# Kernel tuning notes

Measured on AMD Instinct MI355X. Metric: run time of the kernel, lower is better.

## Reference

```python
import jax, jax.numpy as jnp
import numpy as np

B = 8
S_MAX = 1024
H = 12
HD = 64
D = H * HD
DFF = 4 * D
NEG = -1.0e9  # matches Triton kernel's -1000000000.0 mask value


def _layernorm(x, g, b, eps=1e-6):
    mu = jnp.mean(x, axis=-1, keepdims=True)
    var = jnp.mean((x - mu) ** 2, axis=-1, keepdims=True)
    return (x - mu) * jax.lax.rsqrt(var + eps) * g + b


def setup_inputs() -> dict:
    key = jax.random.key(0)
    ks = jax.random.split(key, 12)
    lengths = np.array([1024, 896, 768, 640, 896, 1024, 512, 384], dtype=np.int32)
    assert lengths.max() <= S_MAX and len(lengths) == B
    total = int(lengths.sum())  # 6144
    cu = jnp.asarray(np.concatenate([[0], np.cumsum(lengths)]), dtype=jnp.int32)
    s = 0.02
    return {
        "x": jax.random.normal(ks[0], (total, D), jnp.float32),
        "cu_seqlens": cu,
        "g1": jnp.ones((D,), jnp.float32),
        "beta1": jnp.zeros((D,), jnp.float32),
        "Wqkv": jax.random.normal(ks[1], (D, 3 * D), jnp.float32) * s,
        "bqkv": jnp.zeros((3 * D,), jnp.float32),
        "Wo": jax.random.normal(ks[2], (D, D), jnp.float32) * s,
        "bo": jnp.zeros((D,), jnp.float32),
        "g2": jnp.ones((D,), jnp.float32),
        "beta2": jnp.zeros((D,), jnp.float32),
        "W1": jax.random.normal(ks[3], (D, DFF), jnp.float32) * s,
        "b_fc1": jnp.zeros((DFF,), jnp.float32),
        "W2": jax.random.normal(ks[4], (DFF, D), jnp.float32) * s,
        "b_fc2": jnp.zeros((D,), jnp.float32),
    }


def _ragged_attention(q, k, v, cu_seqlens):
    # q,k,v: [Total, H, HD] packed ragged sequences; cu_seqlens: [B+1] int32
    total = q.shape[0]
    lens = cu_seqlens[1:] - cu_seqlens[:-1]                      # [B]
    s = jnp.arange(S_MAX)
    pad_idx = cu_seqlens[:-1, None] + jnp.minimum(s[None, :], lens[:, None] - 1)  # [B,S]
    valid = s[None, :] < lens[:, None]                           # [B,S]
    qp = q[pad_idx]                                              # [B,S,H,HD]
    kp = k[pad_idx]
    vp = v[pad_idx]
    scale = 1.0 / jnp.sqrt(jnp.float32(HD))
    scores = jnp.einsum("bqhd,bkhd->bhqk", qp, kp) * scale      # [B,H,S,S]
    scores = jnp.where(valid[:, None, None, :], scores, NEG)     # mask invalid keys
    p = jax.nn.softmax(scores, axis=-1)
    op = jnp.einsum("bhqk,bkhd->bqhd", p, vp)                   # [B,S,H,HD]
    # repack to [Total, H, HD]
    tok = jnp.arange(total)
    seg = jnp.searchsorted(cu_seqlens, tok, side="right") - 1    # sequence id per token
    pos = tok - cu_seqlens[seg]
    return op[seg, pos]


def _forward(x, cu_seqlens, g1, beta1, Wqkv, bqkv, Wo, bo, g2, beta2, W1, b_fc1, W2, b_fc2):
    total = x.shape[0]
    qkv = (_layernorm(x, g1, beta1) @ Wqkv + bqkv).reshape(total, 3, H, HD)
    q, k, v = qkv[:, 0], qkv[:, 1], qkv[:, 2]
    attn = _ragged_attention(q, k, v, cu_seqlens).reshape(total, D)
    x = x + (attn @ Wo + bo)                                     # proj_drop/ls1/drop_path identity (eval)
    h = _layernorm(x, g2, beta2)
    m = jax.nn.gelu(h @ W1 + b_fc1, approximate=False)
    return x + (m @ W2 + b_fc2)


def reference(x, cu_seqlens, g1, beta1, Wqkv, bqkv, Wo, bo, g2, beta2, W1, b_fc1, W2, b_fc2):
    return _forward(x, cu_seqlens, g1, beta1, Wqkv, bqkv, Wo, bo, g2, beta2, W1, b_fc1, W2, b_fc2)
```

## Files before the change

kernel.cpp:

```cpp
#include <hip/hip_runtime.h>
#include <hip/hip_bf16.h>
#include <stdint.h>
#include <string.h>

#define D_MODEL 768
#define H_HEADS 12
#define HD_ 64
#define N_QKV 2304

typedef __bf16 bf16x8 __attribute__((ext_vector_type(8)));
typedef float f32x4 __attribute__((ext_vector_type(4)));
typedef __attribute__((address_space(3))) char lds_char;

__device__ __forceinline__ unsigned short f2bfbits(float f) {
  union { float f; unsigned u; } x; x.f = f;
  unsigned r = x.u + 0x7fffu + ((x.u >> 16) & 1u);
  return (unsigned short)(r >> 16);
}

__device__ __forceinline__ unsigned pk2(float a, float b) {
  union { float f; unsigned u; } x, y; x.f = a; y.f = b;
  return ((x.u + 0x8000u) >> 16) | ((y.u + 0x8000u) & 0xffff0000u);
}

__device__ __forceinline__ void gload_lds16(const void* g, void* l) {
  __builtin_amdgcn_global_load_lds(
      (const __attribute__((address_space(1))) unsigned int*)g,
      (__attribute__((address_space(3))) unsigned int*)l, 16, 0, 0);
}

#define DSR(dst, ptr, IMM) \
  asm volatile("ds_read_b128 %0, %1 offset:%2" : "=v"(dst) : "v"(ptr), "n"(IMM))

#define FENCE_() __builtin_amdgcn_sched_barrier(0)
__device__ __forceinline__ void store_sync() {
  FENCE_();
  asm volatile("s_waitcnt lgkmcnt(0)");
  FENCE_();
  __builtin_amdgcn_s_barrier();
  FENCE_();
}

__global__ void transpose_w(const float* __restrict__ in, unsigned short* __restrict__ out,
                            int R, int C) {
  __shared__ float tile[32][33];
  int c0 = blockIdx.x * 32, r0 = blockIdx.y * 32;
  int tx = threadIdx.x, ty = threadIdx.y;
#pragma unroll
  for (int i = 0; i < 32; i += 8)
    tile[ty + i][tx] = in[(size_t)(r0 + ty + i) * C + c0 + tx];
  __syncthreads();
#pragma unroll
  for (int i = 0; i < 32; i += 8)
    out[(size_t)(c0 + ty + i) * R + r0 + tx] = f2bfbits(tile[tx][ty + i]);
}

__global__ void transpose_v(const unsigned short* __restrict__ qkv,
                            unsigned short* __restrict__ vT, int M) {
  __shared__ unsigned short tile[32][33];
  int t0 = blockIdx.x * 32, c0 = blockIdx.y * 32;
  int tx = threadIdx.x, ty = threadIdx.y;
#pragma unroll
  for (int i = 0; i < 32; i += 8)
    tile[ty + i][tx] = qkv[(size_t)(t0 + ty + i) * N_QKV + 1536 + c0 + tx];
  __syncthreads();
  int t = t0 + tx;
  int c = t & 63;
  int kp = ((c >> 5) << 5) | (((c >> 2) & 3) << 3) | (((c >> 4) & 1) << 2) | (c & 3);
  size_t col = (size_t)(t & ~63) + kp;
#pragma unroll
  for (int i = 0; i < 32; i += 8)
    vT[(size_t)(c0 + ty + i) * M + col] = tile[tx][ty + i];
}

__global__ void ln_bf16(const float* __restrict__ x, const float* __restrict__ g,
                        const float* __restrict__ be, unsigned short* __restrict__ out) {
  int row = blockIdx.x;
  const float* xr = x + (size_t)row * D_MODEL;
  int t = threadIdx.x;
  float v0 = xr[t], v1 = xr[t + 256], v2 = xr[t + 512];
  float s = v0 + v1 + v2;
  float s2 = v0 * v0 + v1 * v1 + v2 * v2;
#pragma unroll
  for (int off = 32; off > 0; off >>= 1) {
    s += __shfl_down(s, off, 64);
    s2 += __shfl_down(s2, off, 64);
  }
  __shared__ float red[8];
  int w = t >> 6, lane = t & 63;
  if (lane == 0) { red[w] = s; red[w + 4] = s2; }
  __syncthreads();
  if (t == 0) {
    float a = red[0] + red[1] + red[2] + red[3];
    float b = red[4] + red[5] + red[6] + red[7];
    red[0] = a * (1.0f / 768.0f);
    red[4] = b * (1.0f / 768.0f);
  }
  __syncthreads();
  float mu = red[0];
  float var = red[4] - mu * mu;
  float rs = rsqrtf(var + 1e-6f);
  unsigned short* orow = out + (size_t)row * D_MODEL;
  orow[t]       = f2bfbits((v0 - mu) * rs * g[t]       + be[t]);
  orow[t + 256] = f2bfbits((v1 - mu) * rs * g[t + 256] + be[t + 256]);
  orow[t + 512] = f2bfbits((v2 - mu) * rs * g[t + 512] + be[t + 512]);
}

template <int EPI>
__global__ void __launch_bounds__(256, 3)
gemm_rs(const unsigned short* __restrict__ A,
        const unsigned short* __restrict__ Bt,
        const float* __restrict__ bias,
        const float* __restrict__ res,
        void* __restrict__ outv,
        int M, int N, int K) {
  __shared__ unsigned short lA[2][128 * 32];
  __shared__ unsigned short lB[2][128 * 32];
  int tid = threadIdx.x;
  int w = tid >> 6, lane = tid & 63;
  int id = blockIdx.x;
  int nn = N >> 7, bandM = (M >> 7) >> 3;
  int xcd = id & 7, s = id >> 3;
  int mt = xcd * bandM + s / nn;
  int nt = s - (s / nn) * nn;
  int m0 = mt * 128, n0 = nt * 128;
  int wm = (w >> 1) * 64, wn = (w & 1) * 64;
  f32x4 acc[4][4];
#pragma unroll
  for (int i = 0; i < 4; i++)
#pragma unroll
    for (int j = 0; j < 4; j++) acc[i][j] = (f32x4){0.f, 0.f, 0.f, 0.f};

  int fm = lane & 15, fg = lane >> 4;

  int r0s = w * 16 + (lane >> 2);
  int sc0 = (lane & 3) ^ ((r0s >> 1) & 3);
  const unsigned short* gAs = A + (size_t)(m0 + r0s) * K + sc0 * 8;
  const unsigned short* gBs = Bt + (size_t)(n0 + r0s) * K + sc0 * 8;
  char* lA0 = (char*)&lA[0][0];
  char* lB0 = (char*)&lB[0][0];
  int wo = w * 1024;
  int nk = K >> 5;

  auto stage = [&](int kt, int buf) {
    int kk = kt < nk ? kt : nk - 1;
    int off = kk * 32;
    gload_lds16(gAs + off,                  lA0 + buf * 8192 + wo);
    gload_lds16(gAs + off + (size_t)64 * K, lA0 + buf * 8192 + 4096 + wo);
    gload_lds16(gBs + off,                  lB0 + buf * 8192 + wo);
    gload_lds16(gBs + off + (size_t)64 * K, lB0 + buf * 8192 + 4096 + wo);
  };

  const unsigned aoff0 = (unsigned)((wm + fm) * 64 + ((((wm + fm) >> 1) & 3) ^ fg) * 16);
  const unsigned boff0 = (unsigned)((wn + fm) * 64 + ((((wn + fm) >> 1) & 3) ^ fg) * 16);

  stage(0, 0);
  stage(1, 1);

  for (int k = 0; k < nk; ++k) {
    int cur = k & 1;
    asm volatile("s_waitcnt vmcnt(4)");
    FENCE_();
    __builtin_amdgcn_s_barrier();
    FENCE_();
    bf16x8 af[4], bfr[4];
    const lds_char* pa = (const lds_char*)(lA0 + cur * 8192 + aoff0);
    const lds_char* pb = (const lds_char*)(lB0 + cur * 8192 + boff0);
    DSR(af[0], pa, 0); DSR(af[1], pa, 1024); DSR(af[2], pa, 2048); DSR(af[3], pa, 3072);
    DSR(bfr[0], pb, 0); DSR(bfr[1], pb, 1024); DSR(bfr[2], pb, 2048); DSR(bfr[3], pb, 3072);
    asm volatile("s_waitcnt lgkmcnt(0)");
    FENCE_();
    __builtin_amdgcn_s_barrier();
    FENCE_();
    stage(k + 2, cur);
    FENCE_();
#pragma unroll
    for (int i = 0; i < 4; ++i)
#pragma unroll
      for (int j = 0; j < 4; ++j)
        acc[i][j] = __builtin_amdgcn_mfma_f32_16x16x32_bf16(af[i], bfr[j], acc[i][j], 0, 0, 0);
  }
  asm volatile("s_waitcnt vmcnt(0)");
  FENCE_();

  int er = (lane >> 4) * 4, ec = lane & 15;
#pragma unroll
  for (int i = 0; i < 4; i++) {
#pragma unroll
    for (int j = 0; j < 4; j++) {
      int n = n0 + wn + j * 16 + ec;
      float bv = bias[n];
#pragma unroll
      for (int r = 0; r < 4; r++) {
        int m = m0 + wm + i * 16 + er + r;
        float v = acc[i][j][r] + bv;
        if (EPI == 1) {
          v += res[(size_t)m * N + n];
          ((float*)outv)[(size_t)m * N + n] = v;
        } else {
          if (EPI == 2) v = 0.5f * v * (1.0f + erff(v * 0.70710678118f));
          ((unsigned short*)outv)[(size_t)m * N + n] = f2bfbits(v);
        }
      }
    }
  }
}

template <int EPI>
__global__ void __launch_bounds__(256, 4)
gemm_n64(const unsigned short* __restrict__ A,
         const unsigned short* __restrict__ Bt,
         const float* __restrict__ bias,
         const float* __restrict__ res,
         void* __restrict__ outv,
         int M, int N, int K) {
  __shared__ unsigned short lA[2][128 * 32];
  __shared__ unsigned short lB[2][64 * 32];
  int tid = threadIdx.x;
  int w = tid >> 6, lane = tid & 63;
  int id = blockIdx.x;
  int nn = N >> 6, bandM = (M >> 7) >> 3;
  int xcd = id & 7, s = id >> 3;
  int mt = xcd * bandM + s / nn;
  int nt = s - (s / nn) * nn;
  int m0 = mt * 128, n0 = nt * 64;
  int wm = w * 32;
  f32x4 acc[2][4];
#pragma unroll
  for (int i = 0; i < 2; i++)
#pragma unroll
    for (int j = 0; j < 4; j++) acc[i][j] = (f32x4){0.f, 0.f, 0.f, 0.f};

  int fm = lane & 15, fg = lane >> 4;

  int r0s = w * 16 + (lane >> 2);
  int sc0 = (lane & 3) ^ ((r0s >> 1) & 3);
  const unsigned short* gAs = A + (size_t)(m0 + r0s) * K + sc0 * 8;
  const unsigned short* gBs = Bt + (size_t)(n0 + r0s) * K + sc0 * 8;
  char* lA0 = (char*)&lA[0][0];
  char* lB0 = (char*)&lB[0][0];
  int wo = w * 1024;
  int nk = K >> 5;

  auto stage = [&](int kt, int buf) {
    int kk = kt < nk ? kt : nk - 1;
    int off = kk * 32;
    gload_lds16(gAs + off,                  lA0 + buf * 8192 + wo);
    gload_lds16(gAs + off + (size_t)64 * K, lA0 + buf * 8192 + 4096 + wo);
    gload_lds16(gBs + off,                  lB0 + buf * 4096 + wo);
  };

  const unsigned aoff0 = (unsigned)((wm + fm) * 64 + ((((wm + fm) >> 1) & 3) ^ fg) * 16);
  const unsigned boff0 = (unsigned)(fm * 64 + (((fm >> 1) & 3) ^ fg) * 16);

  stage(0, 0);
  stage(1, 1);

  for (int k = 0; k < nk; ++k) {
    int cur = k & 1;
    asm volatile("s_waitcnt vmcnt(3)");
    FENCE_();
    __builtin_amdgcn_s_barrier();
    FENCE_();
    bf16x8 af[2], bfr[4];
    const lds_char* pa = (const lds_char*)(lA0 + cur * 8192 + aoff0);
    const lds_char* pb = (const lds_char*)(lB0 + cur * 4096 + boff0);
    DSR(af[0], pa, 0); DSR(af[1], pa, 1024);
    DSR(bfr[0], pb, 0); DSR(bfr[1], pb, 1024); DSR(bfr[2], pb, 2048); DSR(bfr[3], pb, 3072);
    asm volatile("s_waitcnt lgkmcnt(0)");
    FENCE_();
    __builtin_amdgcn_s_barrier();
    FENCE_();
    stage(k + 2, cur);
    FENCE_();
#pragma unroll
    for (int i = 0; i < 2; ++i)
#pragma unroll
      for (int j = 0; j < 4; ++j)
        acc[i][j] = __builtin_amdgcn_mfma_f32_16x16x32_bf16(af[i], bfr[j], acc[i][j], 0, 0, 0);
  }
  asm volatile("s_waitcnt vmcnt(0)");
  FENCE_();

  int er = (lane >> 4) * 4, ec = lane & 15;
#pragma unroll
  for (int i = 0; i < 2; i++) {
#pragma unroll
    for (int j = 0; j < 4; j++) {
      int n = n0 + j * 16 + ec;
      float bv = bias[n];
#pragma unroll
      for (int r = 0; r < 4; r++) {
        int m = m0 + wm + i * 16 + er + r;
        float v = acc[i][j][r] + bv;
        if (EPI == 1) {
          v += res[(size_t)m * N + n];
          ((float*)outv)[(size_t)m * N + n] = v;
        } else {
          if (EPI == 2) v = 0.5f * v * (1.0f + erff(v * 0.70710678118f));
          ((unsigned short*)outv)[(size_t)m * N + n] = f2bfbits(v);
        }
      }
    }
  }
}

__global__ void attn_flash4(const unsigned short* __restrict__ qkv,
                            const unsigned short* __restrict__ vT,
                            const int* __restrict__ cu,
                            unsigned short* __restrict__ out, int M) {
  int id = blockIdx.x;
  int qc = id / 96;
  int bh = id - qc * 96;
  int b = bh / 12, h = bh - b * 12;
  int tok0 = cu[b];
  int len = cu[b + 1] - tok0;
  if (qc * 128 >= len) return;

  __shared__ unsigned short lK[2][64 * 64];
  __shared__ unsigned short lVT[2][64 * 64];

  int tid = threadIdx.x, w = tid >> 6, lane = tid & 63;
  int fm = lane & 15, fg = lane >> 4;
  int xm = fm & 7;
  int qbase = qc * 128 + w * 32;

  bf16x8 qf[2][2];
#pragma unroll
  for (int qs = 0; qs < 2; qs++)
#pragma unroll
    for (int kh = 0; kh < 2; kh++)
      qf[qs][kh] = *(const bf16x8*)(qkv + (size_t)(tok0 + qbase + qs * 16 + fm) * N_QKV +
                                    h * 64 + kh * 32 + fg * 8);

  f32x4 Oacc[2][4];
#pragma unroll
  for (int qs = 0; qs < 2; qs++)
#pragma unroll
    for (int dt = 0; dt < 4; dt++) Oacc[qs][dt] = (f32x4){0.f, 0.f, 0.f, 0.f};
  float lrow[2] = {0.f, 0.f};
  const float C2 = 0.18033688011112042f;

  int sr = tid >> 3, sp = tid & 7, sl = sp ^ (sr & 7);
  const unsigned short* kg0 = qkv + D_MODEL + h * 64 + sl * 8;
  const unsigned short* vg0 = vT + (size_t)(h * 64 + sr) * M + tok0 + sl * 8;

  uint4 rk0, rk1, rv0, rv1;
  auto gload = [&](int kt) {
    rk0 = *(const uint4*)(kg0 + (size_t)(tok0 + kt + sr) * N_QKV);
    rk1 = *(const uint4*)(kg0 + (size_t)(tok0 + kt + sr + 32) * N_QKV);
    rv0 = *(const uint4*)(vg0 + kt);
    rv1 = *(const uint4*)(vg0 + (size_t)32 * M + kt);
  };

  int nkt = len >> 6;
  gload(0);
  for (int kt = 0; kt < nkt; kt++) {
    int cur = kt & 1;
    *(uint4*)((char*)&lK[cur][0] + tid * 16) = rk0;
    *(uint4*)((char*)&lK[cur][0] + tid * 16 + 4096) = rk1;
    *(uint4*)((char*)&lVT[cur][0] + tid * 16) = rv0;
    *(uint4*)((char*)&lVT[cur][0] + tid * 16 + 4096) = rv1;
    if (kt + 1 < nkt) gload((kt + 1) * 64);
    store_sync();

    f32x4 s[2][4];
#pragma unroll
    for (int qs = 0; qs < 2; qs++)
#pragma unroll
      for (int t = 0; t < 4; t++) s[qs][t] = (f32x4){0.f, 0.f, 0.f, 0.f};
#pragma unroll
    for (int t = 0; t < 4; t++) {
      bf16x8 kf0 = *(const bf16x8*)&lK[cur][(t * 16 + fm) * 64 + ((fg ^ xm) * 8)];
      bf16x8 kf1 = *(const bf16x8*)&lK[cur][(t * 16 + fm) * 64 + (((4 + fg) ^ xm) * 8)];
#pragma unroll
      for (int qs = 0; qs < 2; qs++) {
        s[qs][t] = __builtin_amdgcn_mfma_f32_16x16x32_bf16(kf0, qf[qs][0], s[qs][t], 0, 0, 0);
        s[qs][t] = __builtin_amdgcn_mfma_f32_16x16x32_bf16(kf1, qf[qs][1], s[qs][t], 0, 0, 0);
      }
    }

    union { bf16x8 v; unsigned u[4]; } af[2][2];
#pragma unroll
    for (int qs = 0; qs < 2; qs++) {
      float ssum = 0.f;
#pragma unroll
      for (int t = 0; t < 4; t++) {
#pragma unroll
        for (int r = 0; r < 4; r++) {
          float p = exp2f(s[qs][t][r] * C2);
          s[qs][t][r] = p;
          ssum += p;
        }
      }
      lrow[qs] += ssum;
      af[qs][0].u[0] = pk2(s[qs][0][0], s[qs][0][1]);
      af[qs][0].u[1] = pk2(s[qs][0][2], s[qs][0][3]);
      af[qs][0].u[2] = pk2(s[qs][1][0], s[qs][1][1]);
      af[qs][0].u[3] = pk2(s[qs][1][2], s[qs][1][3]);
      af[qs][1].u[0] = pk2(s[qs][2][0], s[qs][2][1]);
      af[qs][1].u[1] = pk2(s[qs][2][2], s[qs][2][3]);
      af[qs][1].u[2] = pk2(s[qs][3][0], s[qs][3][1]);
      af[qs][1].u[3] = pk2(s[qs][3][2], s[qs][3][3]);
    }

#pragma unroll
    for (int dt = 0; dt < 4; dt++) {
      bf16x8 vf0 = *(const bf16x8*)&lVT[cur][(dt * 16 + fm) * 64 + ((fg ^ xm) * 8)];
      bf16x8 vf1 = *(const bf16x8*)&lVT[cur][(dt * 16 + fm) * 64 + (((4 + fg) ^ xm) * 8)];
#pragma unroll
      for (int qs = 0; qs < 2; qs++) {
        Oacc[qs][dt] = __builtin_amdgcn_mfma_f32_16x16x32_bf16(af[qs][0].v, vf0, Oacc[qs][dt], 0, 0, 0);
        Oacc[qs][dt] = __builtin_amdgcn_mfma_f32_16x16x32_bf16(af[qs][1].v, vf1, Oacc[qs][dt], 0, 0, 0);
      }
    }
  }

#pragma unroll
  for (int qs = 0; qs < 2; qs++) {
    lrow[qs] += __shfl_xor(lrow[qs], 16, 64);
    lrow[qs] += __shfl_xor(lrow[qs], 32, 64);
    float inv = 1.0f / lrow[qs];
    float ir[4];
#pragma unroll
    for (int r = 0; r < 4; r++) ir[r] = __shfl(inv, fg * 4 + r, 64);
#pragma unroll
    for (int dt = 0; dt < 4; dt++)
#pragma unroll
      for (int r = 0; r < 4; r++)
        out[(size_t)(tok0 + qbase + qs * 16 + fg * 4 + r) * D_MODEL + h * 64 + dt * 16 + fm] =
            f2bfbits(Oacc[qs][dt][r] * ir[r]);
  }
}

extern "C" void kernel_launch(void* const* d_in, const int* in_sizes, int n_in,
                              void* d_out, int out_size, void* d_ws, size_t ws_size,
                              hipStream_t stream) {
  const float* x    = (const float*)d_in[0];
  const int* cu     = (const int*)d_in[1];
  const float* g1   = (const float*)d_in[2];
  const float* be1  = (const float*)d_in[3];
  const float* Wqkv = (const float*)d_in[4];
  const float* bqkv = (const float*)d_in[5];
  const float* Wo   = (const float*)d_in[6];
  const float* bo   = (const float*)d_in[7];
  const float* g2   = (const float*)d_in[8];
  const float* be2  = (const float*)d_in[9];
  const float* W1   = (const float*)d_in[10];
  const float* bfc1 = (const float*)d_in[11];
  const float* W2   = (const float*)d_in[12];
  const float* bfc2 = (const float*)d_in[13];
  float* out = (float*)d_out;
  int M = in_sizes[0] / D_MODEL;

  unsigned short* WqkvT = (unsigned short*)d_ws;
  unsigned short* WoT   = WqkvT + 2304 * 768;
  unsigned short* W1T   = WoT + 768 * 768;
  unsigned short* W2T   = W1T + 3072 * 768;
  unsigned short* bufA  = W2T + 768 * 3072;
  float* x1             = (float*)(bufA + (size_t)M * D_MODEL);
  unsigned short* qkvb  = (unsigned short*)(x1 + (size_t)M * D_MODEL);
  unsigned short* vT = (unsigned short*)x1;

  dim3 b32(32, 8);
  transpose_w<<<dim3(2304 / 32, 768 / 32), b32, 0, stream>>>(Wqkv, WqkvT, 768, 2304);
  transpose_w<<<dim3(768 / 32, 768 / 32), b32, 0, stream>>>(Wo, WoT, 768, 768);
  transpose_w<<<dim3(3072 / 32, 768 / 32), b32, 0, stream>>>(W1, W1T, 768, 3072);
  transpose_w<<<dim3(768 / 32, 3072 / 32), b32, 0, stream>>>(W2, W2T, 3072, 768);

  ln_bf16<<<M, 256, 0, stream>>>(x, g1, be1, bufA);
  gemm_rs<0><<<(2304 / 128) * (M / 128), 256, 0, stream>>>(bufA, WqkvT, bqkv, nullptr, qkvb, M, 2304, 768);
  transpose_v<<<dim3(M / 32, 768 / 32), b32, 0, stream>>>(qkvb, vT, M);
  attn_flash4<<<8 * 96, 256, 0, stream>>>(qkvb, vT, cu, bufA, M);
  gemm_n64<1><<<(768 / 64) * (M / 128), 256, 0, stream>>>(bufA, WoT, bo, x, x1, M, 768, 768);
  ln_bf16<<<M, 256, 0, stream>>>(x1, g2, be2, bufA);
  gemm_rs<2><<<(3072 / 128) * (M / 128), 256, 0, stream>>>(bufA, W1T, bfc1, nullptr, qkvb, M, 3072, 768);
  gemm_n64<1><<<(768 / 64) * (M / 128), 256, 0, stream>>>(qkvb, W2T, bfc2, x1, out, M, 768, 3072);
}
```

Baseline: 351.4 us.

## Replace direct global-to-LDS loads with register-staged prefetch in GEMM main loop

Measured after the change: 344.0 us. 2.1% less time.

```diff
diff --git a/kernel.cpp b/kernel.cpp
--- a/kernel.cpp
+++ b/kernel.cpp
@@ -231,56 +231,87 @@
 #pragma unroll
     for (int j = 0; j < 4; j++) acc[i][j] = (f32x4){0.f, 0.f, 0.f, 0.f};
 
+  int sr = tid >> 2, sc = tid & 3;
+  const unsigned short* gA = A + (size_t)(m0 + sr) * K + sc * 8;
+  const unsigned short* gB = Bt + (size_t)(n0 + sr) * K + sc * 8;
+  int wOff = sr * 64 + ((((sr >> 1) & 3) ^ sc) * 16);
   int fm = lane & 15, fg = lane >> 4;
 
-  int r0s = w * 16 + (lane >> 2);
-  int sc0 = (lane & 3) ^ ((r0s >> 1) & 3);
-  const unsigned short* gAs = A + (size_t)(m0 + r0s) * K + sc0 * 8;
-  const unsigned short* gBs = Bt + (size_t)(n0 + r0s) * K + sc0 * 8;
-  char* lA0 = (char*)&lA[0][0];
-  char* lB0 = (char*)&lB[0][0];
-  int wo = w * 1024;
+  uint4 pA0, pA1, pB0;
+  uint4 qA0, qA1, qB0;
+
   int nk = K >> 5;
-
-  auto stage = [&](int kt, int buf) {
-    int kk = kt < nk ? kt : nk - 1;
-    int off = kk * 32;
-    gload_lds16(gAs + off,                  lA0 + buf * 8192 + wo);
-    gload_lds16(gAs + off + (size_t)64 * K, lA0 + buf * 8192 + 4096 + wo);
-    gload_lds16(gBs + off,                  lB0 + buf * 4096 + wo);
-  };
-
-  const unsigned aoff0 = (unsigned)((wm + fm) * 64 + ((((wm + fm) >> 1) & 3) ^ fg) * 16);
-  const unsigned boff0 = (unsigned)(fm * 64 + (((fm >> 1) & 3) ^ fg) * 16);
-
-  stage(0, 0);
-  stage(1, 1);
-
-  for (int k = 0; k < nk; ++k) {
-    int cur = k & 1;
-    asm volatile("s_waitcnt vmcnt(3)");
-    FENCE_();
-    __builtin_amdgcn_s_barrier();
-    FENCE_();
-    bf16x8 af[2], bfr[4];
-    const lds_char* pa = (const lds_char*)(lA0 + cur * 8192 + aoff0);
-    const lds_char* pb = (const lds_char*)(lB0 + cur * 4096 + boff0);
-    DSR(af[0], pa, 0); DSR(af[1], pa, 1024);
-    DSR(bfr[0], pb, 0); DSR(bfr[1], pb, 1024); DSR(bfr[2], pb, 2048); DSR(bfr[3], pb, 3072);
-    asm volatile("s_waitcnt lgkmcnt(0)");
-    FENCE_();
-    __builtin_amdgcn_s_barrier();
-    FENCE_();
-    stage(k + 2, cur);
-    FENCE_();
-#pragma unroll
-    for (int i = 0; i < 2; ++i)
-#pragma unroll
-      for (int j = 0; j < 4; ++j)
-        acc[i][j] = __builtin_amdgcn_mfma_f32_16x16x32_bf16(af[i], bfr[j], acc[i][j], 0, 0, 0);
-  }
-  asm volatile("s_waitcnt vmcnt(0)");
-  FENCE_();
+  pA0 = *(const uint4*)(gA);
+  pA1 = *(const uint4*)(gA + (size_t)64 * K);
+  pB0 = *(const uint4*)(gB);
+  qA0 = *(const uint4*)(gA + 32);
+  qA1 = *(const uint4*)(gA + (size_t)64 * K + 32);
+  qB0 = *(const uint4*)(gB + 32);
+
+  for (int k = 0; k < nk; k += 2) {
+    {
+      char* la = (char*)&lA[0][0];
+      char* lb = (char*)&lB[0][0];
+      *(uint4*)(la + wOff) = pA0;
+      *(uint4*)(la + wOff + 4096) = pA1;
+      *(uint4*)(lb + wOff) = pB0;
+      if (k + 2 < nk) {
+        int k0 = (k + 2) * 32;
+        pA0 = *(const uint4*)(gA + k0);
+        pA1 = *(const uint4*)(gA + (size_t)64 * K + k0);
+        pB0 = *(const uint4*)(gB + k0);
+      }
+      store_sync();
+      bf16x8 af[2], bfr[4];
+#pragma unroll
+      for (int i = 0; i < 2; i++) {
+        int rr = wm + i * 16 + fm;
+        af[i] = *(const bf16x8*)(la + rr * 64 + ((((rr >> 1) & 3) ^ fg) * 16));
+      }
+#pragma unroll
+      for (int j = 0; j < 4; j++) {
+        int rr = j * 16 + fm;
+        bfr[j] = *(const bf16x8*)(lb + rr * 64 + ((((rr >> 1) & 3) ^ fg) * 16));
+      }
+#pragma unroll
+      for (int i = 0; i < 2; i++)
+#pragma unroll
+        for (int j = 0; j < 4; j++)
+          acc[i][j] = __builtin_amdgcn_mfma_f32_16x16x32_bf16(af[i], bfr[j], acc[i][j], 0, 0, 0);
+      store_sync();
+    }
+    {
+      char* la = (char*)&lA[1][0];
+      char* lb = (char*)&lB[1][0];
+      *(uint4*)(la + wOff) = qA0;
+      *(uint4*)(la + wOff + 4096) = qA1;
+      *(uint4*)(lb + wOff) = qB0;
+      if (k + 3 < nk) {
+        int k0 = (k + 3) * 32;
+        qA0 = *(const uint4*)(gA + k0);
+        qA1 = *(const uint4*)(gA + (size_t)64 * K + k0);
+        qB0 = *(const uint4*)(gB + k0);
+      }
+      store_sync();
+      bf16x8 af[2], bfr[4];
+#pragma unroll
+      for (int i = 0; i < 2; i++) {
+        int rr = wm + i * 16 + fm;
+        af[i] = *(const bf16x8*)(la + rr * 64 + ((((rr >> 1) & 3) ^ fg) * 16));
+      }
+#pragma unroll
+      for (int j = 0; j < 4; j++) {
+        int rr = j * 16 + fm;
+        bfr[j] = *(const bf16x8*)(lb + rr * 64 + ((((rr >> 1) & 3) ^ fg) * 16));
+      }
+#pragma unroll
+      for (int i = 0; i < 2; i++)
+#pragma unroll
+        for (int j = 0; j < 4; j++)
+          acc[i][j] = __builtin_amdgcn_mfma_f32_16x16x32_bf16(af[i], bfr[j], acc[i][j], 0, 0, 0);
+      store_sync();
+    }
+  }
 
   int er = (lane >> 4) * 4, ec = lane & 15;
 #pragma unroll
```
